# Optimization experiments

Hardware: AMD Instinct MI355X
Metric: run time of the kernel (lower is better)

## Reference

```python
import jax, jax.numpy as jnp
import numpy as np

VOCAB, FEAT, NCLS = 50000, 128, 20
N_NODES, N_EDGES = 50000, 1600000
H1, C1 = 8, 8  # conv1: 8 heads x 8 dims


def setup_inputs() -> dict:
    key = jax.random.key(0)
    ks = jax.random.split(key, 12)
    inp = {
        "x_ids": jax.random.randint(ks[0], (N_NODES,), 0, VOCAB),
        "edge_index": jax.random.randint(ks[1], (2, N_EDGES), 0, N_NODES),
        "emb": jax.random.normal(ks[2], (VOCAB, FEAT), jnp.float32) * 0.05,
        "W1": jax.random.normal(ks[3], (FEAT, H1 * C1), jnp.float32) * (1.0 / np.sqrt(FEAT)),
        "a_src1": jax.random.normal(ks[4], (H1, C1), jnp.float32) * 0.1,
        "a_dst1": jax.random.normal(ks[5], (H1, C1), jnp.float32) * 0.1,
        "b1": jnp.zeros((H1 * C1,), jnp.float32),
        "W2": jax.random.normal(ks[6], (H1 * C1, NCLS), jnp.float32) * (1.0 / np.sqrt(H1 * C1)),
        "a_src2": jax.random.normal(ks[7], (1, NCLS), jnp.float32) * 0.1,
        "a_dst2": jax.random.normal(ks[8], (1, NCLS), jnp.float32) * 0.1,
        "b2": jnp.zeros((NCLS,), jnp.float32),
    }
    return inp


def gat_conv(x, src, dst, W, a_src, a_dst, n_nodes):
    """One GATConv layer (PyG semantics, eval mode). Returns [N, H, C]."""
    H, C = a_src.shape
    xp = (x @ W).reshape(n_nodes, H, C)          # projected node feats
    asrc = jnp.sum(xp * a_src, axis=-1)          # [N, H]
    adst = jnp.sum(xp * a_dst, axis=-1)          # [N, H]
    e = jax.nn.leaky_relu(asrc[src] + adst[dst], negative_slope=0.2)  # [E, H]
    # segment softmax over incoming edges of each dst node (self-loops guarantee coverage)
    m = jax.ops.segment_max(e, dst, num_segments=n_nodes)
    p = jnp.exp(e - m[dst])
    s = jax.ops.segment_sum(p, dst, num_segments=n_nodes)
    alpha = p / s[dst]                           # [E, H]
    out = jax.ops.segment_sum(xp[src] * alpha[:, :, None], dst, num_segments=n_nodes)
    return out                                   # [N, H, C]


def reference(x_ids, edge_index, emb, W1, a_src1, a_dst1, b1, W2, a_src2, a_dst2, b2):
    n = x_ids.shape[0]
    loops = jnp.arange(n)
    src = jnp.concatenate([edge_index[0], loops])  # PyG GATConv adds self-loops
    dst = jnp.concatenate([edge_index[1], loops])

    x = emb[x_ids]                                  # embedding lookup, [N, FEAT]
    h = gat_conv(x, src, dst, W1, a_src1, a_dst1, n).reshape(n, -1) + b1  # concat heads
    h = jax.nn.elu(h)
    o = gat_conv(h, src, dst, W2, a_src2, a_dst2, n).mean(axis=1) + b2    # concat=False -> mean
    return jax.nn.log_softmax(o, axis=-1)
```

## Files before the change

### kernel.cpp

```cpp
#include <hip/hip_runtime.h>
#include <cstddef>


#define EPB 2048

typedef float f32x2 __attribute__((ext_vector_type(2)));

__device__ __forceinline__ float lrelu(float x) { return x > 0.f ? x : 0.2f * x; }
__device__ __forceinline__ int iadd(int* p, int v) {
  return __hip_atomic_fetch_add(p, v, __ATOMIC_RELAXED, __HIP_MEMORY_SCOPE_AGENT);
}
__device__ __forceinline__ unsigned f2bf(float f) {
  unsigned int u = __float_as_uint(f);
  u += 0x7FFFu + ((u >> 16) & 1u);
  return u >> 16;
}


__global__ __launch_bounds__(256) void k_bhist(
    const int* __restrict__ ei, int* __restrict__ bhist, int E)
{
  __shared__ int h[256];
  h[threadIdx.x] = 0; __syncthreads();
  for (int e = blockIdx.x * 256 + threadIdx.x; e < E; e += gridDim.x * 256)
    atomicAdd(&h[__builtin_nontemporal_load(&ei[E + e]) >> 8], 1);
  __syncthreads();
  int c = h[threadIdx.x];
  if (c) iadd(&bhist[threadIdx.x], c);
}

__global__ __launch_bounds__(256) void k_bscan(
    const int* __restrict__ bhist, int* __restrict__ bufOffs,
    int* __restrict__ tail, int nb)
{
  __shared__ int sp[256];
  const int tid = threadIdx.x;
  int v = (tid < nb) ? bhist[tid] : 0;
  sp[tid] = v; __syncthreads();
  for (int off = 1; off < 256; off <<= 1) {
    int t = (tid >= off) ? sp[tid - off] : 0;
    __syncthreads();
    sp[tid] += t;
    __syncthreads();
  }
  int excl = sp[tid] - v;
  if (tid < nb) { bufOffs[tid] = excl; tail[tid] = excl; }
  if (tid == 255) bufOffs[nb] = sp[255];
}

__global__ __launch_bounds__(256) void k_part(
    const int* __restrict__ ei, int* __restrict__ tail,
    int* __restrict__ buf, int E)
{
  __shared__ int sPair[EPB];
  __shared__ unsigned char sKey[EPB];
  __shared__ int sHist[256];
  __shared__ int sBase[256];
  const int tid = threadIdx.x;
  sHist[tid] = 0; __syncthreads();
  const int e0 = blockIdx.x * EPB;
  int m = E - e0; if (m > EPB) m = EPB;
  for (int i = tid; i < m; i += 256) {
    int d = __builtin_nontemporal_load(&ei[E + e0 + i]);
    int s = __builtin_nontemporal_load(&ei[e0 + i]);
    sPair[i] = ((d & 255) << 16) | s;
    int b = d >> 8;
    sKey[i] = (unsigned char)b;
    atomicAdd(&sHist[b], 1);
  }
  __syncthreads();
  int c = sHist[tid];
  sBase[tid] = c ? iadd(&tail[tid], c) : 0;
  sHist[tid] = 0;
  __syncthreads();
  for (int i = tid; i < m; i += 256) {
    int b = sKey[i];
    int off = atomicAdd(&sHist[b], 1);
    buf[sBase[b] + off] = sPair[i];
  }
}

__global__ __launch_bounds__(256) void k_coffs_scat(
    const int* __restrict__ buf, const int* __restrict__ bufOffs,
    int* __restrict__ offs, int* __restrict__ csr, int n)
{
  __shared__ int h[256];
  __shared__ int cur[256];
  const int b = blockIdx.x, tid = threadIdx.x;
  const int d = (b << 8) + tid;
  h[tid] = (d < n) ? 1 : 0;
  __syncthreads();
  const int lo = bufOffs[b], hi = bufOffs[b + 1];
  for (int i = lo + tid; i < hi; i += 256)
    atomicAdd(&h[(buf[i] >> 16) & 255], 1);
  __syncthreads();
  const int cnt = h[tid];
  for (int off = 1; off < 256; off <<= 1) {
    int t = (tid >= off) ? h[tid - off] : 0;
    __syncthreads();
    h[tid] += t;
    __syncthreads();
  }
  const int excl = h[tid] - cnt;
  const int base = lo + (b << 8);
  if (d < n) {
    const int o = base + excl;
    offs[d] = o;
    csr[o] = d << 6;
    cur[tid] = o + 1;
    if (d == n - 1) offs[n] = o + cnt;
  }
  __syncthreads();
  for (int i = lo + tid; i < hi; i += 256) {
    int p = buf[i];
    int pos = atomicAdd(&cur[(p >> 16) & 255], 1);
    csr[pos] = (p & 0xFFFF) << 6;
  }
}

__global__ __launch_bounds__(256) void k_embed_proj1(
    const int* __restrict__ x_ids, const float* __restrict__ emb,
    const float* __restrict__ W1, const float* __restrict__ a_dst1,
    unsigned char* __restrict__ xp1f8, float* __restrict__ adst1, int n)
{
  __shared__ float sWT[64 * 132];
  __shared__ float sx[4][2][128];
  for (int i = threadIdx.x; i < 128 * 64; i += 256) {
    int k = i >> 6, c = i & 63;
    sWT[c * 132 + k] = W1[i];
  }
  __syncthreads();
  const int wid = threadIdx.x >> 6;
  const int ln  = threadIdx.x & 63;
  const int ch  = ln;
  const int hh = ch >> 3, cc = ch & 7;
  const float ad = a_dst1[ch];
  const float* wrow = sWT + ch * 132;
  const int half = ln >> 5;
  const int qk   = ln & 31;
  float* myx = &sx[wid][0][0];
  for (int g = 0; g < 4; ++g) {
    const int node0 = blockIdx.x * 32 + g * 8 + wid * 2;
    const int node_s = node0 + half;
    float4 xv = make_float4(0.f, 0.f, 0.f, 0.f);
    if (node_s < n)
      xv = *(const float4*)(emb + (size_t)x_ids[node_s] * 128 + qk * 4);
    *(float4*)(myx + half * 128 + qk * 4) = xv;
    asm volatile("s_waitcnt lgkmcnt(0)" ::: "memory");
    float acc0 = 0.f, acc1 = 0.f;
#pragma unroll 8
    for (int k = 0; k < 128; k += 4) {
      const float4 wv = *(const float4*)(wrow + k);
      const float4 x0 = *(const float4*)(myx + k);
      const float4 x1 = *(const float4*)(myx + 128 + k);
      acc0 = fmaf(x0.x, wv.x, acc0); acc1 = fmaf(x1.x, wv.x, acc1);
      acc0 = fmaf(x0.y, wv.y, acc0); acc1 = fmaf(x1.y, wv.y, acc1);
      acc0 = fmaf(x0.z, wv.z, acc0); acc1 = fmaf(x1.z, wv.z, acc1);
      acc0 = fmaf(x0.w, wv.w, acc0); acc1 = fmaf(x1.w, wv.w, acc1);
    }
    float vd0 = acc0 * ad, vd1 = acc1 * ad;
    vd0 += __shfl_xor(vd0, 1); vd0 += __shfl_xor(vd0, 2); vd0 += __shfl_xor(vd0, 4);
    vd1 += __shfl_xor(vd1, 1); vd1 += __shfl_xor(vd1, 2); vd1 += __shfl_xor(vd1, 4);
    const int node1 = node0 + 1;
    if (node0 < n) {
      unsigned int pk = (unsigned int)__builtin_amdgcn_cvt_pk_fp8_f32(
          acc0 * 16.f, acc0 * 16.f, 0, false);
      xp1f8[(size_t)node0 * 64 + ch] = (unsigned char)pk;
      if (cc == 0) adst1[node0 * 8 + hh] = vd0;
    }
    if (node1 < n) {
      unsigned int pk = (unsigned int)__builtin_amdgcn_cvt_pk_fp8_f32(
          acc1 * 16.f, acc1 * 16.f, 0, false);
      xp1f8[(size_t)node1 * 64 + ch] = (unsigned char)pk;
      if (cc == 0) adst1[node1 * 8 + hh] = vd1;
    }
    asm volatile("s_waitcnt lgkmcnt(0)" ::: "memory");
  }
}

__global__ __launch_bounds__(256) void k_gather1(
    const int* __restrict__ offs, const int* __restrict__ csr,
    const float* __restrict__ a_src1, const float* __restrict__ adst1,
    const unsigned char* __restrict__ xp1f8,
    unsigned char* __restrict__ xp1h, int n)
{
  const int wid = threadIdx.x >> 6;
  const int ln  = threadIdx.x & 63;
  const int eslot = ln >> 3;
  const int h     = ln & 7;
  const int c0    = h << 3;
  const int d = blockIdx.x * 4 + wid;
  if (d >= n) return;
  const float4 a1lo0 = *(const float4*)(a_src1 + c0);
  const float4 a1hi0 = *(const float4*)(a_src1 + c0 + 4);
  const float s0 = a1lo0.x * 0.0625f, s1 = a1lo0.y * 0.0625f;
  const float s2 = a1lo0.z * 0.0625f, s3 = a1lo0.w * 0.0625f;
  const float s4 = a1hi0.x * 0.0625f, s5 = a1hi0.y * 0.0625f;
  const float s6 = a1hi0.z * 0.0625f, s7 = a1hi0.w * 0.0625f;
  const int beg = offs[d], end = offs[d + 1];
  const float adT = adst1[(size_t)d * 8 + h];
  const int hoff = h << 3;
  float a0=0.f,a1=0.f,a2=0.f,a3=0.f,a4=0.f,a5=0.f,a6=0.f,a7=0.f,den=0.f;
#pragma unroll 4
  for (int jb = beg + eslot; jb < end; jb += 8) {
    const int sv = __builtin_nontemporal_load(&csr[jb]);
    const uint2 u = *(const uint2*)(xp1f8 + (unsigned)sv + hoff);
    const f32x2 v01 = __builtin_amdgcn_cvt_pk_f32_fp8((int)u.x, false);
    const f32x2 v23 = __builtin_amdgcn_cvt_pk_f32_fp8((int)u.x, true);
    const f32x2 v45 = __builtin_amdgcn_cvt_pk_f32_fp8((int)u.y, false);
    const f32x2 v67 = __builtin_amdgcn_cvt_pk_f32_fp8((int)u.y, true);
    float dot = v01.x * s0;
    dot = fmaf(v01.y, s1, dot); dot = fmaf(v23.x, s2, dot);
    dot = fmaf(v23.y, s3, dot); dot = fmaf(v45.x, s4, dot);
    dot = fmaf(v45.y, s5, dot); dot = fmaf(v67.x, s6, dot);
    dot = fmaf(v67.y, s7, dot);
    const float p = __expf(lrelu(dot + adT));
    a0 = fmaf(p, v01.x, a0); a1 = fmaf(p, v01.y, a1);
    a2 = fmaf(p, v23.x, a2); a3 = fmaf(p, v23.y, a3);
    a4 = fmaf(p, v45.x, a4); a5 = fmaf(p, v45.y, a5);
    a6 = fmaf(p, v67.x, a6); a7 = fmaf(p, v67.y, a7);
    den += p;
  }
#pragma unroll
  for (int off = 8; off < 64; off <<= 1) {
    a0 += __shfl_xor(a0, off); a1 += __shfl_xor(a1, off);
    a2 += __shfl_xor(a2, off); a3 += __shfl_xor(a3, off);
    a4 += __shfl_xor(a4, off); a5 += __shfl_xor(a5, off);
    a6 += __shfl_xor(a6, off); a7 += __shfl_xor(a7, off);
    den += __shfl_xor(den, off);
  }
  if (eslot == 0) {
    const float inv16 = 1.f / den * 0.0625f;
    uint4 w;
    w.x = f2bf(a0 * inv16) | (f2bf(a1 * inv16) << 16);
    w.y = f2bf(a2 * inv16) | (f2bf(a3 * inv16) << 16);
    w.z = f2bf(a4 * inv16) | (f2bf(a5 * inv16) << 16);
    w.w = f2bf(a6 * inv16) | (f2bf(a7 * inv16) << 16);
    *(uint4*)(xp1h + (size_t)d * 128 + (h << 4)) = w;
  }
}

__global__ __launch_bounds__(256) void k_proj2(
    const unsigned char* __restrict__ xp1h, const float* __restrict__ b1,
    const float* __restrict__ W2, const float* __restrict__ a_src2,
    const float* __restrict__ a_dst2,
    unsigned int* __restrict__ xp2b, float* __restrict__ adst2, int n)
{
  __shared__ float sW[64 * 20];
  for (int i = threadIdx.x; i < 64 * 20; i += 256) sW[i] = W2[i];
  __syncthreads();
  const int node = blockIdx.x * 64 + (threadIdx.x >> 2);
  const int part = threadIdx.x & 3;
  if (node >= n) return;
  const int k0 = part * 16;
  const uint4 u0 = *(const uint4*)(xp1h + (size_t)node * 128 + k0 * 2);
  const uint4 u1 = *(const uint4*)(xp1h + (size_t)node * 128 + k0 * 2 + 16);
  float hv[16];
  {
    const unsigned uu[8] = {u0.x,u0.y,u0.z,u0.w,u1.x,u1.y,u1.z,u1.w};
#pragma unroll
    for (int j = 0; j < 8; ++j) {
      float t0 = __uint_as_float(uu[j] << 16)        + b1[k0 + 2*j];
      float t1 = __uint_as_float(uu[j] & 0xFFFF0000u) + b1[k0 + 2*j + 1];
      hv[2*j]   = t0 > 0.f ? t0 : expm1f(t0);
      hv[2*j+1] = t1 > 0.f ? t1 : expm1f(t1);
    }
  }
  float acc[20];
#pragma unroll
  for (int c = 0; c < 20; ++c) acc[c] = 0.f;
#pragma unroll
  for (int j = 0; j < 16; ++j) {
    const float hj = hv[j];
    const float* wr = sW + (k0 + j) * 20;
#pragma unroll
    for (int c = 0; c < 20; ++c) acc[c] = fmaf(hj, wr[c], acc[c]);
  }
#pragma unroll
  for (int c = 0; c < 20; ++c) {
    acc[c] += __shfl_xor(acc[c], 1);
    acc[c] += __shfl_xor(acc[c], 2);
  }
  float vs = 0.f, vd = 0.f;
#pragma unroll
  for (int c = 0; c < 20; ++c) {
    vs = fmaf(acc[c], a_src2[c], vs);
    vd = fmaf(acc[c], a_dst2[c], vd);
  }
  const int p5 = part * 5;
  uint4 w;
  w.x = f2bf(acc[p5 + 0]) | (f2bf(acc[p5 + 1]) << 16);
  w.y = f2bf(acc[p5 + 2]) | (f2bf(acc[p5 + 3]) << 16);
  w.z = f2bf(acc[p5 + 4]);
  w.w = __float_as_uint(vs);
  *(uint4*)(xp2b + (size_t)node * 16 + part * 4) = w;
  if (part == 0) adst2[node] = vd;
}

__global__ __launch_bounds__(256) void k_gather2(
    const int* __restrict__ offs, const int* __restrict__ csr,
    const float* __restrict__ adst2,
    const unsigned char* __restrict__ xp2c, const float* __restrict__ b2,
    float* __restrict__ out, int n)
{
  const int wid = threadIdx.x >> 6, ln = threadIdx.x & 63;
  const int eslot = ln >> 2, q = ln & 3;
  const int d = blockIdx.x * 4 + wid;
  if (d >= n) return;
  const int beg = offs[d], end = offs[d + 1];
  const float adT = adst2[d];
  const int qoff = q << 4;
  float a0=0.f,a1=0.f,a2=0.f,a3=0.f,a4=0.f,den=0.f;
#pragma unroll 2
  for (int jb = beg + eslot; jb < end; jb += 16) {
    const int sv = __builtin_nontemporal_load(&csr[jb]);
    const uint4 u = *(const uint4*)(xp2c + (unsigned)sv + qoff);
    const float p = __expf(lrelu(__uint_as_float(u.w) + adT));
    a0 = fmaf(p, __uint_as_float(u.x << 16), a0);
    a1 = fmaf(p, __uint_as_float(u.x & 0xFFFF0000u), a1);
    a2 = fmaf(p, __uint_as_float(u.y << 16), a2);
    a3 = fmaf(p, __uint_as_float(u.y & 0xFFFF0000u), a3);
    a4 = fmaf(p, __uint_as_float(u.z << 16), a4);
    den += p;
  }
#pragma unroll
  for (int off = 4; off < 64; off <<= 1) {
    a0 += __shfl_xor(a0, off); a1 += __shfl_xor(a1, off);
    a2 += __shfl_xor(a2, off); a3 += __shfl_xor(a3, off);
    a4 += __shfl_xor(a4, off);
    den += __shfl_xor(den, off);
  }
  const float inv = 1.f / den;
  const int c5 = q * 5;
  float o[5];
  float mx;
  {
    o[0] = a0 * inv + b2[c5 + 0];
    o[1] = a1 * inv + b2[c5 + 1];
    o[2] = a2 * inv + b2[c5 + 2];
    o[3] = a3 * inv + b2[c5 + 3];
    o[4] = a4 * inv + b2[c5 + 4];
    mx = fmaxf(fmaxf(fmaxf(o[0], o[1]), fmaxf(o[2], o[3])), o[4]);
  }
  mx = fmaxf(mx, __shfl_xor(mx, 1));
  mx = fmaxf(mx, __shfl_xor(mx, 2));
  float ss = __expf(o[0] - mx) + __expf(o[1] - mx) + __expf(o[2] - mx)
           + __expf(o[3] - mx) + __expf(o[4] - mx);
  ss += __shfl_xor(ss, 1);
  ss += __shfl_xor(ss, 2);
  const float lse = mx + __logf(ss);
  if (eslot == 0) {
#pragma unroll
    for (int j = 0; j < 5; ++j)
      out[(size_t)d * 20 + c5 + j] = o[j] - lse;
  }
}


extern "C" void kernel_launch(void* const* d_in, const int* in_sizes, int n_in,
                              void* d_out, int out_size, void* d_ws, size_t ws_size,
                              hipStream_t stream)
{
  const int*   x_ids  = (const int*)d_in[0];
  const int*   ei     = (const int*)d_in[1];
  const float* emb    = (const float*)d_in[2];
  const float* W1     = (const float*)d_in[3];
  const float* a_src1 = (const float*)d_in[4];
  const float* a_dst1 = (const float*)d_in[5];
  const float* b1     = (const float*)d_in[6];
  const float* W2     = (const float*)d_in[7];
  const float* a_src2 = (const float*)d_in[8];
  const float* a_dst2 = (const float*)d_in[9];
  const float* b2     = (const float*)d_in[10];
  float* out = (float*)d_out;

  const int n = in_sizes[0];
  const int E = in_sizes[1] / 2;
  const int nb = (n + 255) >> 8;

  char* base = (char*)d_ws;
  size_t r0 = (size_t)n * 64;
  if ((size_t)E * 4 > r0) r0 = (size_t)E * 4;
  r0 = (r0 + 255) & ~(size_t)255;
  unsigned char* xp1f8 = (unsigned char*)base;
  int*   buf   = (int*)base;
  float* adst1 = (float*)(base + r0);
  unsigned char* xp1h = (unsigned char*)(adst1 + (size_t)n * 8);
  unsigned int* xp2b = (unsigned int*)(xp1h + (size_t)n * 128);
  float* adst2 = (float*)(xp2b + (size_t)n * 16);
  int*   offs   = (int*)(adst2 + (size_t)n);
  int*   bhist  = offs + n + 1;
  int*   bufOffs= bhist + 256;
  int*   tail   = bufOffs + 257;
  int*   csr    = tail + 256;

  hipMemsetAsync(bhist, 0, 256 * sizeof(int), stream);

  k_bhist<<<256, 256, 0, stream>>>(ei, bhist, E);
  k_bscan<<<1, 256, 0, stream>>>(bhist, bufOffs, tail, nb);
  k_part<<<(E + EPB - 1) / EPB, 256, 0, stream>>>(ei, tail, buf, E);
  k_coffs_scat<<<nb, 256, 0, stream>>>(buf, bufOffs, offs, csr, n);

  k_embed_proj1<<<(n + 31) / 32, 256, 0, stream>>>(
      x_ids, emb, W1, a_dst1, xp1f8, adst1, n);

  k_gather1<<<(n + 3) / 4, 256, 0, stream>>>(
      offs, csr, a_src1, adst1, xp1f8, xp1h, n);

  k_proj2<<<(n + 63) / 64, 256, 0, stream>>>(
      xp1h, b1, W2, a_src2, a_dst2, xp2b, adst2, n);

  k_gather2<<<(n + 3) / 4, 256, 0, stream>>>(
      offs, csr, adst2, (const unsigned char*)xp2b, b2, out, n);
}
```

Baseline: 201.5 us.

## Replace histogram memset and atomics with per-block partials; prefetch embedding rows

The bucket histogram now writes per-block partial counts to a 64x256 array that the scan kernel sums. This removes the memset launch and the global atomics, at the cost of fewer histogram blocks and more reads in the single-block scan. Separately, the embed/projection kernel software-prefetches the next group's embedding row into registers while the current group is computed, to hide gather latency at the cost of more register use.

```diff
diff --git a/kernel.cpp b/kernel.cpp
--- a/kernel.cpp
+++ b/kernel.cpp
@@ -3,6 +3,7 @@
 
 
 #define EPB 2048
+#define NHB 64
 
 typedef float f32x2 __attribute__((ext_vector_type(2)));
 
@@ -18,24 +19,25 @@
 
 
 __global__ __launch_bounds__(256) void k_bhist(
-    const int* __restrict__ ei, int* __restrict__ bhist, int E)
+    const int* __restrict__ ei, int* __restrict__ bhistP, int E)
 {
   __shared__ int h[256];
   h[threadIdx.x] = 0; __syncthreads();
-  for (int e = blockIdx.x * 256 + threadIdx.x; e < E; e += gridDim.x * 256)
+  for (int e = blockIdx.x * 256 + threadIdx.x; e < E; e += NHB * 256)
     atomicAdd(&h[__builtin_nontemporal_load(&ei[E + e]) >> 8], 1);
   __syncthreads();
-  int c = h[threadIdx.x];
-  if (c) iadd(&bhist[threadIdx.x], c);
+  bhistP[(blockIdx.x << 8) + threadIdx.x] = h[threadIdx.x];
 }
 
 __global__ __launch_bounds__(256) void k_bscan(
-    const int* __restrict__ bhist, int* __restrict__ bufOffs,
+    const int* __restrict__ bhistP, int* __restrict__ bufOffs,
     int* __restrict__ tail, int nb)
 {
   __shared__ int sp[256];
   const int tid = threadIdx.x;
-  int v = (tid < nb) ? bhist[tid] : 0;
+  int v = 0;
+#pragma unroll 8
+  for (int b = 0; b < NHB; ++b) v += bhistP[(b << 8) + tid];
   sp[tid] = v; __syncthreads();
   for (int off = 1; off < 256; off <<= 1) {
     int t = (tid >= off) ? sp[tid - off] : 0;
@@ -139,14 +141,22 @@
   const int half = ln >> 5;
   const int qk   = ln & 31;
   float* myx = &sx[wid][0][0];
-  for (int g = 0; g < 4; ++g) {
-    const int node0 = blockIdx.x * 32 + g * 8 + wid * 2;
-    const int node_s = node0 + half;
-    float4 xv = make_float4(0.f, 0.f, 0.f, 0.f);
+  float4 xv = make_float4(0.f, 0.f, 0.f, 0.f);
+  {
+    const int node_s = blockIdx.x * 32 + wid * 2 + half;
     if (node_s < n)
       xv = *(const float4*)(emb + (size_t)x_ids[node_s] * 128 + qk * 4);
+  }
+  for (int g = 0; g < 4; ++g) {
     *(float4*)(myx + half * 128 + qk * 4) = xv;
+    float4 xnext = make_float4(0.f, 0.f, 0.f, 0.f);
+    if (g < 3) {
+      const int node_s = blockIdx.x * 32 + (g + 1) * 8 + wid * 2 + half;
+      if (node_s < n)
+        xnext = *(const float4*)(emb + (size_t)x_ids[node_s] * 128 + qk * 4);
+    }
     asm volatile("s_waitcnt lgkmcnt(0)" ::: "memory");
+    const int node0 = blockIdx.x * 32 + g * 8 + wid * 2;
     float acc0 = 0.f, acc1 = 0.f;
 #pragma unroll 8
     for (int k = 0; k < 128; k += 4) {
@@ -175,6 +185,7 @@
       if (cc == 0) adst1[node1 * 8 + hh] = vd1;
     }
     asm volatile("s_waitcnt lgkmcnt(0)" ::: "memory");
+    xv = xnext;
   }
 }
 
@@ -389,15 +400,13 @@
   unsigned int* xp2b = (unsigned int*)(xp1h + (size_t)n * 128);
   float* adst2 = (float*)(xp2b + (size_t)n * 16);
   int*   offs   = (int*)(adst2 + (size_t)n);
-  int*   bhist  = offs + n + 1;
-  int*   bufOffs= bhist + 256;
+  int*   bhistP = offs + n + 1;
+  int*   bufOffs= bhistP + NHB * 256;
   int*   tail   = bufOffs + 257;
   int*   csr    = tail + 256;
 
-  hipMemsetAsync(bhist, 0, 256 * sizeof(int), stream);
-
-  k_bhist<<<256, 256, 0, stream>>>(ei, bhist, E);
-  k_bscan<<<1, 256, 0, stream>>>(bhist, bufOffs, tail, nb);
+  k_bhist<<<NHB, 256, 0, stream>>>(ei, bhistP, E);
+  k_bscan<<<1, 256, 0, stream>>>(bhistP, bufOffs, tail, nb);
   k_part<<<(E + EPB - 1) / EPB, 256, 0, stream>>>(ei, tail, buf, E);
   k_coffs_scat<<<nb, 256, 0, stream>>>(buf, bufOffs, offs, csr, n);
 
```

Result: slower. 218.6 us (+8.5%).
